# Kernel optimization log

Hardware: AMD Instinct MI355X
Metric: run time of the kernel (lower is better)

The kernel has to match this reference:

```python
import jax, jax.numpy as jnp
import numpy as np
import math

# ---- real-basis Wigner 3j via nullspace of rotation generators ----

def _su2_gen(l):
    m = np.arange(-l, l + 1)
    jz = np.diag(m).astype(complex)
    jp = np.zeros((2 * l + 1, 2 * l + 1), complex)
    for i, mm in enumerate(m[:-1]):
        jp[i + 1, i] = math.sqrt(l * (l + 1) - mm * (mm + 1))
    jm = jp.conj().T
    return (jp + jm) / 2, (jp - jm) / 2j, jz


def _c2r(l):
    # complex -> real spherical-harmonic change of basis
    U = np.zeros((2 * l + 1, 2 * l + 1), complex)
    U[l, l] = 1.0
    s = 1 / math.sqrt(2)
    for m in range(1, l + 1):
        U[l + m, l + m] = (-1) ** m * s
        U[l + m, l - m] = s
        U[l - m, l - m] = 1j * s
        U[l - m, l + m] = -1j * (-1) ** m * s
    return U


def _real_gens(l):
    U = _c2r(l)
    return [np.real(U @ (-1j * J) @ U.conj().T) for J in _su2_gen(l)]


_W3J_CACHE = {}

def _w3j(l1, l2, l3):
    key = (l1, l2, l3)
    if key in _W3J_CACHE:
        return _W3J_CACHE[key]
    X1, X2, X3 = _real_gens(l1), _real_gens(l2), _real_gens(l3)
    d1, d2, d3 = 2 * l1 + 1, 2 * l2 + 1, 2 * l3 + 1
    I1, I2, I3 = np.eye(d1), np.eye(d2), np.eye(d3)
    blocks = []
    for a in range(3):
        K = (np.kron(np.kron(X1[a], I2), I3)
             + np.kron(np.kron(I1, X2[a]), I3)
             + np.kron(np.kron(I1, I2), X3[a]))
        blocks.append(K)
    M = np.concatenate(blocks, 0)
    _, _, Vh = np.linalg.svd(M)
    v = Vh[-1]
    if v[np.argmax(np.abs(v))] < 0:
        v = -v
    w = (v / np.linalg.norm(v)).reshape(d1, d2, d3)
    _W3J_CACHE[key] = w
    return w


# ---- replicate WeightedTensorProduct.__init__ layout logic ----

def _build(ls1, ls2, ls_out):
    dim = lambda ls: sum(2 * l + 1 for l in ls)
    d1, d2, do = dim(ls1), dim(ls2), dim(ls_out)
    lmax2 = max(ls2)
    max_l3 = max(ls_out) + 1
    layout = {}
    idx1 = 0
    for l1 in ls1:
        idx2 = 0
        for l2 in ls2:
            for l3 in range(abs(l1 - l2), min(l1 + l2 + 1, max_l3)):
                layout.setdefault(l3, []).append((l1, l2, idx1 * d2 + idx2))
            idx2 += 2 * l2 + 1
        idx1 += 2 * l1 + 1
    l3s = sorted(layout)
    cbh = sum((2 * l3 + 1) * len(layout[l3]) for l3 in l3s)
    cb = np.zeros((cbh, d1 * d2), np.float32)
    row = 0
    for l3 in l3s:
        layout[l3] = sorted(layout[l3], key=lambda x: x[0] * lmax2 + x[1])
        for (l1, l2, col) in layout[l3]:
            w = _w3j(l1, l2, l3) * math.sqrt(2 * l3 + 1)  # (2l1+1, 2l2+1, 2l3+1)
            for m1 in range(2 * l1 + 1):
                cb[row:row + 2 * l3 + 1, col + m1 * d2: col + m1 * d2 + 2 * l2 + 1] = w[m1].T
            row += 2 * l3 + 1
    # weight-tying mask (one scalar weight per (out-irrep, cb-path) pair)
    out_mult = {}
    for l in ls_out:
        out_mult[l] = out_mult.get(l, 0) + 1
    rows_idx, cols_idx = [], []
    row_idx, widx = 0, 0
    for ol3 in sorted(out_mult):
        for _ in range(out_mult[ol3]):
            col_idx = 0
            for l3 in l3s:
                for _m in range(len(layout[l3])):
                    if ol3 == l3:
                        for m in range(2 * l3 + 1):
                            rows_idx.append((row_idx + m) * cbh + col_idx + m)
                            cols_idx.append(widx)
                        widx += 1
                    col_idx += 2 * l3 + 1
            row_idx += 2 * ol3 + 1
    return cb, np.array(rows_idx, np.int32), np.array(cols_idx, np.int32), widx, do, cbh


def setup_inputs() -> dict:
    LS = [0] * 8 + [1] * 8 + [2] * 4  # dim = 52, for in1, in2 and out
    cb, rows, cols, nw, do, H = _build(LS, LS, LS)
    d = sum(2 * l + 1 for l in LS)
    rng = np.random.default_rng(0)
    w = rng.standard_normal(nw).astype(np.float32)
    Wf = np.zeros(do * H, np.float32)
    Wf[rows] = w[cols]
    B = 4096
    k1, k2 = jax.random.split(jax.random.key(0))
    return {
        "in1": jax.random.normal(k1, (B, d), jnp.float32),
        "in2": jax.random.normal(k2, (B, d), jnp.float32),
        "cb_matrix": jnp.asarray(cb),                  # [H, d*d]
        "weight_matrix": jnp.asarray(Wf.reshape(do, H)),  # [do, H]
    }


def reference(in1, in2, cb_matrix, weight_matrix):
    # out = (W @ C @ outer^T)^T  ==  outer @ C^T @ W^T
    B = in1.shape[0]
    outer = (in1[:, :, None] * in2[:, None, :]).reshape(B, -1)  # [B, d1*d2]
    z = outer @ cb_matrix.T                                     # [B, cb_height]
    return z @ weight_matrix.T                                  # [B, dim_out]
```

## Files before the change

### kernel.cpp

```cpp
#include <hip/hip_runtime.h>
#include <hip/hip_bf16.h>

#define D    52
#define DD   2704
#define HH   2000
#define DO   52
#define KP   3328
#define NO   64
#define KS   4
#define KT_TOTAL (KP/32)
#define KT_PER   (KT_TOTAL/KS)
#define MG   16
#define KCH  128
#define WHP  2048

typedef __attribute__((ext_vector_type(8))) short short8;
typedef __attribute__((ext_vector_type(4))) float f32x4;

#define WB_OFF    0
#define WB_BYTES  (NO * WHP * 2)
#define MTP_OFF   (WB_OFF + WB_BYTES)
#define MTP_BYTES (MG * DD * NO * 4)
#define MTT_OFF   (MTP_OFF + MTP_BYTES)
#define MTT_BYTES (NO * KP * 2)
#define OUTP_OFF  (MTT_OFF + MTT_BYTES)
#define OUTP_BYTES (KS * 4096 * NO * 4)

static __device__ __forceinline__ unsigned short f2bf(float f) {
    __hip_bfloat16 h = __float2bfloat16(f);
    return __builtin_bit_cast(unsigned short, h);
}

__global__ __launch_bounds__(256) void k_packw(
    const float* __restrict__ W, unsigned short* __restrict__ Wb) {
    int idx = blockIdx.x * 256 + threadIdx.x;
    if (idx >= NO * WHP) return;
    int o = idx >> 11, h = idx & (WHP - 1);
    float v = (o < DO && h < HH) ? W[o * HH + h] : 0.f;
    Wb[idx] = f2bf(v);
}

__global__ __launch_bounds__(256) void k_mgemm(
    const float* __restrict__ cb, const unsigned short* __restrict__ Wb,
    float* __restrict__ mtp) {
    __shared__ float shAT[64][33];
    int lane = threadIdx.x & 63;
    int w    = __builtin_amdgcn_readfirstlane(threadIdx.x >> 6);
    int r    = lane & 15;
    int kg   = lane >> 4;
    int ij0  = blockIdx.x * 64;
    int g    = blockIdx.y;

    f32x4 acc[4];
#pragma unroll
    for (int nt = 0; nt < 4; ++nt) acc[nt] = (f32x4){0.f, 0.f, 0.f, 0.f};

    int srow = threadIdx.x >> 6;
    int scol = threadIdx.x & 63;
    int sij  = ij0 + scol;
    bool ijv = (sij < DD);

#pragma unroll
    for (int kt = 0; kt < KCH / 32; ++kt) {
        int h0 = g * KCH + kt * 32;
        __syncthreads();
#pragma unroll
        for (int p = 0; p < 8; ++p) {
            int row = srow + p * 4;
            int h = h0 + row;
            float v = (h < HH && ijv) ? cb[(size_t)h * DD + sij] : 0.f;
            shAT[scol][row] = v;
        }
        __syncthreads();

        int myij = w * 16 + r;
        short8 a;
#pragma unroll
        for (int e = 0; e < 8; ++e)
            a[e] = (short)f2bf(shAT[myij][kg * 8 + e]);
#pragma unroll
        for (int nt = 0; nt < 4; ++nt) {
            short8 b = *reinterpret_cast<const short8*>(
                Wb + (size_t)(nt * 16 + r) * WHP + g * KCH + kt * 32 + kg * 8);
            acc[nt] = __builtin_amdgcn_mfma_f32_16x16x32_bf16(a, b, acc[nt], 0, 0, 0);
        }
    }

#pragma unroll
    for (int nt = 0; nt < 4; ++nt) {
#pragma unroll
        for (int q = 0; q < 4; ++q) {
            int ij = ij0 + w * 16 + kg * 4 + q;
            if (ij < DD)
                mtp[((size_t)g * DD + ij) * NO + nt * 16 + r] = acc[nt][q];
        }
    }
}

__global__ __launch_bounds__(256) void k_reduce_pack(
    const float* __restrict__ mtp, unsigned short* __restrict__ mtT) {
    __shared__ float sh[D][NO + 1];
    int i = blockIdx.x;

    for (int t = threadIdx.x; t < D * NO; t += 256) {
        int row = t >> 6, o = t & 63;
        size_t base = (size_t)(i * D + row) * NO + o;
        float s = 0.f;
#pragma unroll
        for (int g = 0; g < MG; ++g) s += mtp[(size_t)g * DD * NO + base];
        sh[row][o] = s;
    }
    __syncthreads();

    int j  = threadIdx.x & 63;
    int o0 = threadIdx.x >> 6;
    for (int o = o0; o < NO; o += 4) {
        float v = (j < D) ? sh[j][o] : 0.f;
        mtT[(size_t)o * KP + i * 64 + j] = f2bf(v);
    }
}

__global__ __launch_bounds__(256) void k_main_mfma(
    const float* __restrict__ in1, const float* __restrict__ in2,
    const unsigned short* __restrict__ mtT, float* __restrict__ outp) {
    __shared__ float sh1[16][53];
    __shared__ float sh2[16][68];

    int lane = threadIdx.x & 63;
    int wv   = __builtin_amdgcn_readfirstlane(threadIdx.x >> 6);
    int b0   = blockIdx.x * 16;
    int ks   = blockIdx.y;
    int o0   = wv * 16;

    for (int t = threadIdx.x; t < 16 * 64; t += 256) {
        int r = t >> 6, j = t & 63;
        sh2[r][j] = (j < D) ? in2[(size_t)(b0 + r) * D + j] : 0.f;
    }
    for (int t = threadIdx.x; t < 16 * D; t += 256) {
        int r = t / D, i = t - r * D;
        sh1[r][i] = in1[(size_t)(b0 + r) * D + i];
    }
    __syncthreads();

    int r   = lane & 15;
    int kg  = lane >> 4;
    int oc  = o0 + r;
    const unsigned short* bp = mtT + (size_t)oc * KP + ks * KT_PER * 32 + kg * 8;

    f32x4 acc = {0.f, 0.f, 0.f, 0.f};
#pragma unroll 2
    for (int t = 0; t < KT_PER; ++t) {
        int kt    = ks * KT_PER + t;
        int i     = kt >> 1;
        int j0    = (kt & 1) * 32 + kg * 8;
        float f1  = sh1[r][i];
        short8 a;
#pragma unroll
        for (int e = 0; e < 8; ++e)
            a[e] = (short)f2bf(f1 * sh2[r][j0 + e]);
        short8 b = *reinterpret_cast<const short8*>(bp + (size_t)t * 32);
        acc = __builtin_amdgcn_mfma_f32_16x16x32_bf16(a, b, acc, 0, 0, 0);
    }

#pragma unroll
    for (int q = 0; q < 4; ++q) {
        int row = kg * 4 + q;
        outp[((size_t)ks * 4096 + b0 + row) * NO + o0 + r] = acc[q];
    }
}

__global__ __launch_bounds__(256) void k_out(
    const float* __restrict__ outp, float* __restrict__ out, int B) {
    int idx = blockIdx.x * 256 + threadIdx.x;
    if (idx >= B * DO) return;
    int b = idx / DO, o = idx - b * DO;
    float s = 0.f;
#pragma unroll
    for (int g = 0; g < KS; ++g) s += outp[((size_t)g * B + b) * NO + o];
    out[idx] = s;
}

extern "C" void kernel_launch(void* const* d_in, const int* in_sizes, int n_in,
                              void* d_out, int out_size, void* d_ws, size_t ws_size,
                              hipStream_t stream) {
    const float* in1 = (const float*)d_in[0];
    const float* in2 = (const float*)d_in[1];
    const float* cb  = (const float*)d_in[2];
    const float* W   = (const float*)d_in[3];
    float* out = (float*)d_out;

    int B = in_sizes[0] / D;

    char* ws = (char*)d_ws;
    unsigned short* Wb   = (unsigned short*)(ws + WB_OFF);
    float*          mtp  = (float*)(ws + MTP_OFF);
    unsigned short* mtT  = (unsigned short*)(ws + MTT_OFF);
    float*          outp = (float*)(ws + OUTP_OFF);

    hipLaunchKernelGGL(k_packw, dim3((NO * WHP + 255) / 256), dim3(256), 0,
                       stream, W, Wb);
    hipLaunchKernelGGL(k_mgemm, dim3((DD + 63) / 64, MG), dim3(256), 0,
                       stream, cb, Wb, mtp);
    hipLaunchKernelGGL(k_reduce_pack, dim3(D), dim3(256), 0,
                       stream, mtp, mtT);
    hipLaunchKernelGGL(k_main_mfma, dim3(B / 16, KS), dim3(256), 0,
                       stream, in1, in2, mtT, outp);
    hipLaunchKernelGGL(k_out, dim3((B * DO + 255) / 256), dim3(256), 0,
                       stream, outp, out, B);
}
```

Measured before the change: 119.4 us.

## Transpose M-GEMM output and pack main-GEMM B operand in MFMA tile order

The cb·W precompute GEMM now swaps operands so its partial results are stored o-major with ij contiguous, which makes the per-group stores coalesced. The split-K reduction becomes a widely parallel kernel (a grid over k and o instead of 52 blocks) that writes the bf16 matrix in a tile-blocked layout. In that layout each 32-wide k-tile holds all 64 outputs contiguously, so the main kernel's B-fragment loads are contiguous per tile. The sh2 row padding also changes from 68 to 69 to reduce LDS bank conflicts. The goal is to cut uncoalesced traffic and low parallelism in the prep kernels, with no change to the arithmetic.

Result: faster. 106.6 us (-10.7%).

```diff
diff --git a/kernel.cpp b/kernel.cpp
--- a/kernel.cpp
+++ b/kernel.cpp
@@ -17,13 +17,13 @@
 typedef __attribute__((ext_vector_type(8))) short short8;
 typedef __attribute__((ext_vector_type(4))) float f32x4;
 
-#define WB_OFF    0
-#define WB_BYTES  (NO * WHP * 2)
-#define MTP_OFF   (WB_OFF + WB_BYTES)
-#define MTP_BYTES (MG * DD * NO * 4)
-#define MTT_OFF   (MTP_OFF + MTP_BYTES)
-#define MTT_BYTES (NO * KP * 2)
-#define OUTP_OFF  (MTT_OFF + MTT_BYTES)
+#define WB_OFF     0
+#define WB_BYTES   (NO * WHP * 2)
+#define MTP_OFF    (WB_OFF + WB_BYTES)
+#define MTP_BYTES  (MG * NO * DD * 4)
+#define MTB_OFF    (MTP_OFF + MTP_BYTES)
+#define MTB_BYTES  (KT_TOTAL * NO * 32 * 2)
+#define OUTP_OFF   (MTB_OFF + MTB_BYTES)
 #define OUTP_BYTES (KS * 4096 * NO * 4)
 
 static __device__ __forceinline__ unsigned short f2bf(float f) {
@@ -53,7 +53,7 @@
 
     f32x4 acc[4];
 #pragma unroll
-    for (int nt = 0; nt < 4; ++nt) acc[nt] = (f32x4){0.f, 0.f, 0.f, 0.f};
+    for (int mt = 0; mt < 4; ++mt) acc[mt] = (f32x4){0.f, 0.f, 0.f, 0.f};
 
     int srow = threadIdx.x >> 6;
     int scol = threadIdx.x & 63;
@@ -73,58 +73,50 @@
         }
         __syncthreads();
 
-        int myij = w * 16 + r;
-        short8 a;
+        short8 bf;
 #pragma unroll
         for (int e = 0; e < 8; ++e)
-            a[e] = (short)f2bf(shAT[myij][kg * 8 + e]);
-#pragma unroll
-        for (int nt = 0; nt < 4; ++nt) {
-            short8 b = *reinterpret_cast<const short8*>(
-                Wb + (size_t)(nt * 16 + r) * WHP + g * KCH + kt * 32 + kg * 8);
-            acc[nt] = __builtin_amdgcn_mfma_f32_16x16x32_bf16(a, b, acc[nt], 0, 0, 0);
+            bf[e] = (short)f2bf(shAT[w * 16 + r][kg * 8 + e]);
+#pragma unroll
+        for (int mt = 0; mt < 4; ++mt) {
+            short8 a = *reinterpret_cast<const short8*>(
+                Wb + (size_t)(mt * 16 + r) * WHP + g * KCH + kt * 32 + kg * 8);
+            acc[mt] = __builtin_amdgcn_mfma_f32_16x16x32_bf16(a, bf, acc[mt], 0, 0, 0);
         }
     }
 
-#pragma unroll
-    for (int nt = 0; nt < 4; ++nt) {
-#pragma unroll
-        for (int q = 0; q < 4; ++q) {
-            int ij = ij0 + w * 16 + kg * 4 + q;
-            if (ij < DD)
-                mtp[((size_t)g * DD + ij) * NO + nt * 16 + r] = acc[nt][q];
+    int ij = ij0 + w * 16 + r;
+    if (ij < DD) {
+#pragma unroll
+        for (int mt = 0; mt < 4; ++mt) {
+#pragma unroll
+            for (int q = 0; q < 4; ++q) {
+                int o = mt * 16 + kg * 4 + q;
+                mtp[((size_t)g * NO + o) * DD + ij] = acc[mt][q];
+            }
         }
     }
 }
 
-__global__ __launch_bounds__(256) void k_reduce_pack(
-    const float* __restrict__ mtp, unsigned short* __restrict__ mtT) {
-    __shared__ float sh[D][NO + 1];
-    int i = blockIdx.x;
-
-    for (int t = threadIdx.x; t < D * NO; t += 256) {
-        int row = t >> 6, o = t & 63;
-        size_t base = (size_t)(i * D + row) * NO + o;
-        float s = 0.f;
-#pragma unroll
-        for (int g = 0; g < MG; ++g) s += mtp[(size_t)g * DD * NO + base];
-        sh[row][o] = s;
-    }
-    __syncthreads();
-
-    int j  = threadIdx.x & 63;
-    int o0 = threadIdx.x >> 6;
-    for (int o = o0; o < NO; o += 4) {
-        float v = (j < D) ? sh[j][o] : 0.f;
-        mtT[(size_t)o * KP + i * 64 + j] = f2bf(v);
-    }
+__global__ __launch_bounds__(256) void k_reduce_mtb(
+    const float* __restrict__ mtp, unsigned short* __restrict__ mtB) {
+    int k = blockIdx.x * 256 + threadIdx.x;
+    int o = blockIdx.y;
+    int i = k >> 6, j = k & 63;
+    float s = 0.f;
+    if (j < D) {
+        size_t base = (size_t)o * DD + i * D + j;
+#pragma unroll
+        for (int g = 0; g < MG; ++g) s += mtp[(size_t)g * (NO * DD) + base];
+    }
+    mtB[((size_t)(k >> 5) * NO + o) * 32 + ((k >> 3) & 3) * 8 + (k & 7)] = f2bf(s);
 }
 
 __global__ __launch_bounds__(256) void k_main_mfma(
     const float* __restrict__ in1, const float* __restrict__ in2,
-    const unsigned short* __restrict__ mtT, float* __restrict__ outp) {
+    const unsigned short* __restrict__ mtB, float* __restrict__ outp) {
     __shared__ float sh1[16][53];
-    __shared__ float sh2[16][68];
+    __shared__ float sh2[16][69];
 
     int lane = threadIdx.x & 63;
     int wv   = __builtin_amdgcn_readfirstlane(threadIdx.x >> 6);
@@ -142,23 +134,23 @@
     }
     __syncthreads();
 
-    int r   = lane & 15;
-    int kg  = lane >> 4;
-    int oc  = o0 + r;
-    const unsigned short* bp = mtT + (size_t)oc * KP + ks * KT_PER * 32 + kg * 8;
+    int r  = lane & 15;
+    int kg = lane >> 4;
+    const unsigned short* bp =
+        mtB + ((size_t)(ks * KT_PER) * NO + o0 + r) * 32 + kg * 8;
 
     f32x4 acc = {0.f, 0.f, 0.f, 0.f};
 #pragma unroll 2
     for (int t = 0; t < KT_PER; ++t) {
-        int kt    = ks * KT_PER + t;
-        int i     = kt >> 1;
-        int j0    = (kt & 1) * 32 + kg * 8;
-        float f1  = sh1[r][i];
+        int kt   = ks * KT_PER + t;
+        int i    = kt >> 1;
+        int j0   = (kt & 1) * 32 + kg * 8;
+        float f1 = sh1[r][i];
         short8 a;
 #pragma unroll
         for (int e = 0; e < 8; ++e)
             a[e] = (short)f2bf(f1 * sh2[r][j0 + e]);
-        short8 b = *reinterpret_cast<const short8*>(bp + (size_t)t * 32);
+        short8 b = *reinterpret_cast<const short8*>(bp + (size_t)t * (NO * 32));
         acc = __builtin_amdgcn_mfma_f32_16x16x32_bf16(a, b, acc, 0, 0, 0);
     }
 
@@ -194,17 +186,17 @@
     char* ws = (char*)d_ws;
     unsigned short* Wb   = (unsigned short*)(ws + WB_OFF);
     float*          mtp  = (float*)(ws + MTP_OFF);
-    unsigned short* mtT  = (unsigned short*)(ws + MTT_OFF);
+    unsigned short* mtB  = (unsigned short*)(ws + MTB_OFF);
     float*          outp = (float*)(ws + OUTP_OFF);
 
     hipLaunchKernelGGL(k_packw, dim3((NO * WHP + 255) / 256), dim3(256), 0,
                        stream, W, Wb);
     hipLaunchKernelGGL(k_mgemm, dim3((DD + 63) / 64, MG), dim3(256), 0,
                        stream, cb, Wb, mtp);
-    hipLaunchKernelGGL(k_reduce_pack, dim3(D), dim3(256), 0,
-                       stream, mtp, mtT);
+    hipLaunchKernelGGL(k_reduce_mtb, dim3(KP / 256, NO), dim3(256), 0,
+                       stream, mtp, mtB);
     hipLaunchKernelGGL(k_main_mfma, dim3(B / 16, KS), dim3(256), 0,
-                       stream, in1, in2, mtT, outp);
+                       stream, in1, in2, mtB, outp);
     hipLaunchKernelGGL(k_out, dim3((B * DO + 255) / 256), dim3(256), 0,
                        stream, outp, out, B);
 }
```
